# Kernel optimization log

Measured on AMD Instinct MI355X. Metric: run time of the kernel, lower is better.

The kernel has to match this reference:

```python
import jax, jax.numpy as jnp
import numpy as np


def _to_complex(x):
    # trailing axis holds (real, imag)
    return x[..., 0] + 1j * x[..., 1]


def _nufft2c(img, omega, csm):
    """Exact type-2 non-uniform DFT with coil sensitivities (reference for nufft2c_torch).

    img:   (H, W) real or complex image
    omega: (2, M) k-space coords in cycles/pixel, in [-0.5, 0.5]
    csm:   (C, H, W) complex coil sensitivity maps
    returns (C, M) complex k-space, centered & orthonormal-style 1/sqrt(HW) scaling.
    """
    H, W = img.shape
    y = jnp.arange(H, dtype=jnp.float32) - H / 2.0  # centered pixel coords
    z = jnp.arange(W, dtype=jnp.float32) - W / 2.0
    ey = jnp.exp(-2j * jnp.pi * omega[0][:, None] * y[None, :])  # (M, H)
    ez = jnp.exp(-2j * jnp.pi * omega[1][:, None] * z[None, :])  # (M, W)
    sim = csm * img[None, :, :].astype(csm.dtype)                # (C, H, W)
    tmp = jnp.einsum('chw,mw->cmh', sim, ez)                     # (C, M, H)
    k = jnp.einsum('cmh,mh->cm', tmp, ey) / np.float32(np.sqrt(H * W))
    return k


def setup_inputs() -> dict:
    key = jax.random.key(0)
    k0, k1, k2, k3, k4 = jax.random.split(key, 5)
    H = W = 300
    C = 4       # coils
    M = 4096    # non-Cartesian k-space samples
    img_pred = jax.random.normal(k0, (H, W, 1), jnp.float32)
    kdata = jax.random.normal(k1, (1, C, M, 2), jnp.float32)
    all_omega = jax.random.uniform(k2, (1, 2, M), jnp.float32) - 0.5  # cycles/pixel
    all_dcomp = jax.random.uniform(k3, (1, M), jnp.float32)
    all_csm = jax.random.normal(k4, (C, H, W, 2), jnp.float32)
    return {
        'img_pred': img_pred,
        'kdata': kdata,
        'all_omega': all_omega,
        'all_dcomp': all_dcomp,
        'all_csm': all_csm,
    }


def reference(img_pred, kdata, all_omega, all_dcomp, all_csm):
    Ncontrast = 1
    csm = _to_complex(all_csm)   # (C, H, W)
    kd = _to_complex(kdata)      # (Ncontrast, C, M)
    two_pi = jnp.float32(2.0 * np.pi)
    # radial k-space weighting, (Ncontrast, M)
    weight = jnp.sqrt((all_omega[:, 0, :] * two_pi) ** 2 +
                      (all_omega[:, 1, :] * two_pi) ** 2) + 1.0
    loss = jnp.float32(0.0)
    for ii in range(Ncontrast):
        img = img_pred[:, :, ii]                       # (H, W)
        ksp = _nufft2c(img, all_omega[ii], csm)        # (C, M)
        d = weight[ii][None, :] * (ksp - kd[ii])       # weighted complex residual
        # MSELoss over view_as_real == mean over all real & imag components
        loss = loss + jnp.mean(jnp.stack([d.real, d.imag]) ** 2)
    return loss
```

## Files before the change

### kernel.cpp

```cpp
#include <hip/hip_runtime.h>
#include <math.h>

#define HH 300
#define WW 300
#define CC 4
#define MM 4096
#define KP 640
#define CSTRIDE 384
#define MP (CC*CSTRIDE)
#define NP 8192
#define BK 128
#define NRB (MP/128)

typedef __attribute__((ext_vector_type(4))) float f32x4;
typedef __attribute__((ext_vector_type(4))) int int4v;
typedef __attribute__((ext_vector_type(8))) int int8v;
typedef const __attribute__((address_space(1))) void g_void;
typedef __attribute__((address_space(3))) void l_void;

#define TWO_PI 6.283185307179586f

__device__ __forceinline__ float aval(const float* img, const float* csm,
                                      int c, int h, int k) {
    if (k >= 2 * WW) return 0.0f;
    int w = (k < WW) ? k : k - WW;
    float im = img[h * WW + w];
    const float* cs = csm + (((size_t)c * HH + h) * WW + w) * 2;
    return ((k < WW) ? cs[0] : cs[1]) * im;
}

__device__ __forceinline__ float bval(const float* omega, int n, int k) {
    if (k >= 2 * WW) return 0.0f;
    int m = n & (MM - 1);
    int part = n >> 12;
    int w = (k < WW) ? k : k - WW;
    float om1 = omega[MM + m];
    float s, c;
    __sincosf(TWO_PI * om1 * (float)(w - 150), &s, &c);
    float ezr = c, ezi = -s;
    return (part == 0) ? ((k < WW) ? ezr : -ezi) : ((k < WW) ? ezi : ezr);
}

__global__ __launch_bounds__(256) void prep_kernel(
    const float* __restrict__ img, const float* __restrict__ csm,
    const float* __restrict__ omega, ushort* __restrict__ A,
    ushort* __restrict__ B, float* __restrict__ out)
{
    const int bid = blockIdx.x;
    if (bid == 0 && threadIdx.x == 0) out[0] = 0.0f;
    const int ABLK = (MP * KP / 2) / 256;
    if (bid < ABLK) {
        int idx = bid * 256 + threadIdx.x;
        int row = idx / (KP / 2);
        int k   = (idx - row * (KP / 2)) * 2;
        int c = row / CSTRIDE;
        int h = row - c * CSTRIDE;
        float v0 = 0.0f, v1 = 0.0f;
        if (h < HH) { v0 = aval(img, csm, c, h, k); v1 = aval(img, csm, c, h, k + 1); }
        int pk = __builtin_amdgcn_cvt_pk_fp8_f32(v0, v1, 0, false);
        A[idx] = (ushort)pk;
    } else {
        int idx = (bid - ABLK) * 256 + threadIdx.x;
        int n = idx / (KP / 2);
        int k = (idx - n * (KP / 2)) * 2;
        float v0 = bval(omega, n, k);
        float v1 = bval(omega, n, k + 1);
        int pk = __builtin_amdgcn_cvt_pk_fp8_f32(v0, v1, 0, false);
        B[idx] = (ushort)pk;
    }
}

__global__ __launch_bounds__(256) void gemm_kernel(
    const unsigned char* __restrict__ A, const unsigned char* __restrict__ B,
    const float* __restrict__ omega, float2* __restrict__ P)
{
    __shared__ unsigned char As[128 * BK];
    __shared__ unsigned char Bs[128 * BK];
    __shared__ float2 red[128];

    const int t    = threadIdx.x;
    const int wave = t >> 6;
    const int ln   = t & 63;
    const int row0 = blockIdx.y * 128;
    const int col0 = blockIdx.x * 128;
    const int wr = wave >> 1, wc = wave & 1;
    const int lr = ln & 15;
    const int lq = ln >> 4;

    if (t < 128) red[t] = make_float2(0.0f, 0.0f);

    const int srow  = t >> 3;
    const int cphys = (t >> 1) & 3;
    const int half  = t & 1;
    const int sgoff = ((cphys ^ (srow & 3)) << 5) + (half << 4);

    f32x4 acc[4][4] = {};

    for (int k0 = 0; k0 < KP; k0 += BK) {
        #pragma unroll
        for (int p = 0; p < 4; ++p) {
            const unsigned char* gA = A + (size_t)(row0 + p * 32 + srow) * KP + k0 + sgoff;
            const unsigned char* gB = B + (size_t)(col0 + p * 32 + srow) * KP + k0 + sgoff;
            __builtin_amdgcn_global_load_lds((g_void*)gA, (l_void*)(As + p * 4096 + t * 16), 16, 0, 0);
            __builtin_amdgcn_global_load_lds((g_void*)gB, (l_void*)(Bs + p * 4096 + t * 16), 16, 0, 0);
        }
        __syncthreads();

        int8v a[4], b[4];
        #pragma unroll
        for (int i = 0; i < 4; ++i) {
            const int r = wr * 64 + i * 16 + lr;
            const unsigned char* pA = As + r * BK + ((lq ^ (lr & 3)) << 5);
            int4v lo = *(const int4v*)pA;
            int4v hi = *(const int4v*)(pA + 16);
            a[i] = __builtin_shufflevector(lo, hi, 0, 1, 2, 3, 4, 5, 6, 7);
        }
        #pragma unroll
        for (int j = 0; j < 4; ++j) {
            const int r = wc * 64 + j * 16 + lr;
            const unsigned char* pB = Bs + r * BK + ((lq ^ (lr & 3)) << 5);
            int4v lo = *(const int4v*)pB;
            int4v hi = *(const int4v*)(pB + 16);
            b[j] = __builtin_shufflevector(lo, hi, 0, 1, 2, 3, 4, 5, 6, 7);
        }
        #pragma unroll
        for (int i = 0; i < 4; ++i)
            #pragma unroll
            for (int j = 0; j < 4; ++j)
                acc[i][j] = __builtin_amdgcn_mfma_scale_f32_16x16x128_f8f6f4(
                    a[i], b[j], acc[i][j], 0, 0,
                    0, 0x7f7f7f7f, 0, 0x7f7f7f7f);
        __syncthreads();
    }

    const int c  = row0 / CSTRIDE;
    const int h0 = row0 - c * CSTRIDE;

    #pragma unroll
    for (int j = 0; j < 4; ++j) {
        const int jcol = wc * 64 + j * 16 + lr;
        const int m = (col0 + jcol) & (MM - 1);
        const float om0 = omega[m];
        float ss, sc;
        __sincosf(TWO_PI * om0, &ss, &sc);
        const float str = sc, sti = -ss;
        float pr = 0.0f, pi = 0.0f;
        #pragma unroll
        for (int i = 0; i < 4; ++i) {
            const int hb = h0 + wr * 64 + i * 16 + lq * 4;
            float sn, cs;
            __sincosf(TWO_PI * om0 * (float)(hb - 150), &sn, &cs);
            float er = cs, ei = -sn;
            #pragma unroll
            for (int r = 0; r < 4; ++r) {
                const float v = acc[i][j][r];
                pr = fmaf(v, er, pr);
                pi = fmaf(v, ei, pi);
                float nr = er * str - ei * sti;
                ei = er * sti + ei * str;
                er = nr;
            }
        }
        pr += __shfl_down(pr, 32); pi += __shfl_down(pi, 32);
        pr += __shfl_down(pr, 16); pi += __shfl_down(pi, 16);
        if (lq == 0) {
            atomicAdd(&red[jcol].x, pr);
            atomicAdd(&red[jcol].y, pi);
        }
    }
    __syncthreads();

    if (t < 128) {
        const int rb = row0 >> 7;
        P[(size_t)rb * NP + col0 + t] = red[t];
    }
}

__global__ __launch_bounds__(256) void loss_kernel(
    const float2* __restrict__ P, const float* __restrict__ kdata,
    const float* __restrict__ omega, float* __restrict__ out)
{
    const int t = blockIdx.x * 256 + threadIdx.x;
    const int c = t >> 12;
    const int m = t & (MM - 1);

    float kr = 0.0f, ki = 0.0f;
    #pragma unroll
    for (int q = 0; q < 3; ++q) {
        const int rb = 3 * c + q;
        float2 p0 = P[(size_t)rb * NP + m];
        float2 p1 = P[(size_t)rb * NP + m + MM];
        kr += p0.x - p1.y;
        ki += p0.y + p1.x;
    }
    kr *= (1.0f / 300.0f);
    ki *= (1.0f / 300.0f);

    const float om0 = omega[m];
    const float om1 = omega[MM + m];
    const size_t kidx = ((size_t)c * MM + m) * 2;
    const float kdr = kdata[kidx];
    const float kdi = kdata[kidx + 1];
    const float w0 = om0 * TWO_PI, w1 = om1 * TWO_PI;
    const float wg = sqrtf(w0 * w0 + w1 * w1) + 1.0f;
    const float dr = wg * (kr - kdr);
    const float di = wg * (ki - kdi);
    float val = (dr * dr + di * di) * (1.0f / (2.0f * CC * MM));

    #pragma unroll
    for (int off = 32; off > 0; off >>= 1) val += __shfl_down(val, off);
    if ((threadIdx.x & 63) == 0) atomicAdd(out, val);
}

extern "C" void kernel_launch(void* const* d_in, const int* in_sizes, int n_in,
                              void* d_out, int out_size, void* d_ws, size_t ws_size,
                              hipStream_t stream) {
    const float* img   = (const float*)d_in[0];
    const float* kdata = (const float*)d_in[1];
    const float* omega = (const float*)d_in[2];
    const float* csm   = (const float*)d_in[4];
    float* out = (float*)d_out;

    unsigned char* Aws = (unsigned char*)d_ws;
    unsigned char* Bws = (unsigned char*)d_ws + (1u << 20);
    float2*        Pws = (float2*)((char*)d_ws + (8u << 20));

    const int ablk = (MP * KP / 2) / 256;
    const int bblk = (NP * KP / 2) / 256;
    prep_kernel<<<ablk + bblk, 256, 0, stream>>>(img, csm, omega,
                                                 (ushort*)Aws, (ushort*)Bws, out);
    gemm_kernel<<<dim3(NP / 128, MP / 128), 256, 0, stream>>>(Aws, Bws, omega, Pws);
    loss_kernel<<<(CC * MM) / 256, 256, 0, stream>>>(Pws, kdata, omega, out);
}
```

Measured before the change: 91.56 us.

## Fuse loss into GEMM via last-block reduction, dedupe B prep sincos, remap blocks per XCD

The separate loss kernel is removed. The last GEMM block to finish, found with an atomic counter and threadfence, now reduces all partial products and writes the loss, which saves a launch and the output atomics. B-matrix prep computes each sincos once and writes all four real/imag variants of both parts, so transcendental work drops by about 4x. The GEMM grid is flattened to 1D and remapped so blocks on the same XCD share column tiles for L2 locality. The cost is a serial tail where a single block reduces 16K elements.

```diff
diff --git a/kernel.cpp b/kernel.cpp
--- a/kernel.cpp
+++ b/kernel.cpp
@@ -11,6 +11,7 @@
 #define NP 8192
 #define BK 128
 #define NRB (MP/128)
+#define NBLK ((NP/128)*(MP/128))
 
 typedef __attribute__((ext_vector_type(4))) float f32x4;
 typedef __attribute__((ext_vector_type(4))) int int4v;
@@ -29,25 +30,13 @@
     return ((k < WW) ? cs[0] : cs[1]) * im;
 }
 
-__device__ __forceinline__ float bval(const float* omega, int n, int k) {
-    if (k >= 2 * WW) return 0.0f;
-    int m = n & (MM - 1);
-    int part = n >> 12;
-    int w = (k < WW) ? k : k - WW;
-    float om1 = omega[MM + m];
-    float s, c;
-    __sincosf(TWO_PI * om1 * (float)(w - 150), &s, &c);
-    float ezr = c, ezi = -s;
-    return (part == 0) ? ((k < WW) ? ezr : -ezi) : ((k < WW) ? ezi : ezr);
-}
-
 __global__ __launch_bounds__(256) void prep_kernel(
     const float* __restrict__ img, const float* __restrict__ csm,
     const float* __restrict__ omega, ushort* __restrict__ A,
-    ushort* __restrict__ B, float* __restrict__ out)
+    unsigned char* __restrict__ B, int* __restrict__ counter)
 {
     const int bid = blockIdx.x;
-    if (bid == 0 && threadIdx.x == 0) out[0] = 0.0f;
+    if (bid == 0 && threadIdx.x == 0) *counter = 0;
     const int ABLK = (MP * KP / 2) / 256;
     if (bid < ABLK) {
         int idx = bid * 256 + threadIdx.x;
@@ -61,28 +50,52 @@
         A[idx] = (ushort)pk;
     } else {
         int idx = (bid - ABLK) * 256 + threadIdx.x;
-        int n = idx / (KP / 2);
-        int k = (idx - n * (KP / 2)) * 2;
-        float v0 = bval(omega, n, k);
-        float v1 = bval(omega, n, k + 1);
-        int pk = __builtin_amdgcn_cvt_pk_fp8_f32(v0, v1, 0, false);
-        B[idx] = (ushort)pk;
+        int m  = idx / 160;
+        int wp = idx - m * 160;
+        unsigned char* r0 = B + (size_t)m * KP;
+        unsigned char* r1 = B + (size_t)(m + MM) * KP;
+        if (wp < 150) {
+            int w = wp * 2;
+            float om1 = omega[MM + m];
+            float s0, c0, s1, c1;
+            __sincosf(TWO_PI * om1 * (float)(w - 150), &s0, &c0);
+            __sincosf(TWO_PI * om1 * (float)(w - 149), &s1, &c1);
+            ushort rr = (ushort)__builtin_amdgcn_cvt_pk_fp8_f32(c0, c1, 0, false);
+            ushort ii = (ushort)__builtin_amdgcn_cvt_pk_fp8_f32(-s0, -s1, 0, false);
+            ushort ni = (ushort)__builtin_amdgcn_cvt_pk_fp8_f32(s0, s1, 0, false);
+            *(ushort*)(r0 + w)       = rr;
+            *(ushort*)(r0 + WW + w)  = ni;
+            *(ushort*)(r1 + w)       = ii;
+            *(ushort*)(r1 + WW + w)  = rr;
+        } else {
+            int z = (wp - 150) * 4;
+            *(unsigned int*)(r0 + 600 + z) = 0u;
+            *(unsigned int*)(r1 + 600 + z) = 0u;
+        }
     }
 }
 
 __global__ __launch_bounds__(256) void gemm_kernel(
     const unsigned char* __restrict__ A, const unsigned char* __restrict__ B,
-    const float* __restrict__ omega, float2* __restrict__ P)
+    const float* __restrict__ omega, const float* __restrict__ kdata,
+    float2* __restrict__ P, int* __restrict__ counter, float* __restrict__ out)
 {
     __shared__ unsigned char As[128 * BK];
     __shared__ unsigned char Bs[128 * BK];
     __shared__ float2 red[128];
+    __shared__ float wred[4];
+    __shared__ int lastflag;
 
     const int t    = threadIdx.x;
     const int wave = t >> 6;
     const int ln   = t & 63;
-    const int row0 = blockIdx.y * 128;
-    const int col0 = blockIdx.x * 128;
+
+    const int bid = blockIdx.x;
+    const int xcd = bid & 7;
+    const int sub = bid >> 3;
+    const int row0 = (sub >> 3) * 128;
+    const int col0 = (xcd * 8 + (sub & 7)) * 128;
+
     const int wr = wave >> 1, wc = wave & 1;
     const int lr = ln & 15;
     const int lq = ln >> 4;
@@ -174,42 +187,48 @@
         const int rb = row0 >> 7;
         P[(size_t)rb * NP + col0 + t] = red[t];
     }
-}
-
-__global__ __launch_bounds__(256) void loss_kernel(
-    const float2* __restrict__ P, const float* __restrict__ kdata,
-    const float* __restrict__ omega, float* __restrict__ out)
-{
-    const int t = blockIdx.x * 256 + threadIdx.x;
-    const int c = t >> 12;
-    const int m = t & (MM - 1);
-
-    float kr = 0.0f, ki = 0.0f;
+    __syncthreads();
+
+    if (t == 0) {
+        __threadfence();
+        int old = atomicAdd(counter, 1);
+        lastflag = (old == NBLK - 1);
+    }
+    __syncthreads();
+    if (!lastflag) return;
+    __threadfence();
+
+    float vsum = 0.0f;
+    for (int idx = t; idx < CC * MM; idx += 256) {
+        const int cc = idx >> 12;
+        const int m  = idx & (MM - 1);
+        float kr = 0.0f, ki = 0.0f;
+        #pragma unroll
+        for (int q = 0; q < 3; ++q) {
+            const int rb = 3 * cc + q;
+            float2 p0 = P[(size_t)rb * NP + m];
+            float2 p1 = P[(size_t)rb * NP + m + MM];
+            kr += p0.x - p1.y;
+            ki += p0.y + p1.x;
+        }
+        kr *= (1.0f / 300.0f);
+        ki *= (1.0f / 300.0f);
+        const float o0 = omega[m];
+        const float o1 = omega[MM + m];
+        const size_t kidx = ((size_t)cc * MM + m) * 2;
+        const float kdr = kdata[kidx];
+        const float kdi = kdata[kidx + 1];
+        const float w0 = o0 * TWO_PI, w1 = o1 * TWO_PI;
+        const float wg = sqrtf(w0 * w0 + w1 * w1) + 1.0f;
+        const float dr = wg * (kr - kdr);
+        const float di = wg * (ki - kdi);
+        vsum += (dr * dr + di * di) * (1.0f / (2.0f * CC * MM));
+    }
     #pragma unroll
-    for (int q = 0; q < 3; ++q) {
-        const int rb = 3 * c + q;
-        float2 p0 = P[(size_t)rb * NP + m];
-        float2 p1 = P[(size_t)rb * NP + m + MM];
-        kr += p0.x - p1.y;
-        ki += p0.y + p1.x;
-    }
-    kr *= (1.0f / 300.0f);
-    ki *= (1.0f / 300.0f);
-
-    const float om0 = omega[m];
-    const float om1 = omega[MM + m];
-    const size_t kidx = ((size_t)c * MM + m) * 2;
-    const float kdr = kdata[kidx];
-    const float kdi = kdata[kidx + 1];
-    const float w0 = om0 * TWO_PI, w1 = om1 * TWO_PI;
-    const float wg = sqrtf(w0 * w0 + w1 * w1) + 1.0f;
-    const float dr = wg * (kr - kdr);
-    const float di = wg * (ki - kdi);
-    float val = (dr * dr + di * di) * (1.0f / (2.0f * CC * MM));
-
-    #pragma unroll
-    for (int off = 32; off > 0; off >>= 1) val += __shfl_down(val, off);
-    if ((threadIdx.x & 63) == 0) atomicAdd(out, val);
+    for (int off = 32; off > 0; off >>= 1) vsum += __shfl_down(vsum, off);
+    if (ln == 0) wred[wave] = vsum;
+    __syncthreads();
+    if (t == 0) out[0] = wred[0] + wred[1] + wred[2] + wred[3];
 }
 
 extern "C" void kernel_launch(void* const* d_in, const int* in_sizes, int n_in,
@@ -224,11 +243,11 @@
     unsigned char* Aws = (unsigned char*)d_ws;
     unsigned char* Bws = (unsigned char*)d_ws + (1u << 20);
     float2*        Pws = (float2*)((char*)d_ws + (8u << 20));
+    int*           cnt = (int*)((char*)d_ws + (16u << 20));
 
     const int ablk = (MP * KP / 2) / 256;
-    const int bblk = (NP * KP / 2) / 256;
+    const int bblk = (MM * 160) / 256;
     prep_kernel<<<ablk + bblk, 256, 0, stream>>>(img, csm, omega,
-                                                 (ushort*)Aws, (ushort*)Bws, out);
-    gemm_kernel<<<dim3(NP / 128, MP / 128), 256, 0, stream>>>(Aws, Bws, omega, Pws);
-    loss_kernel<<<(CC * MM) / 256, 256, 0, stream>>>(Pws, kdata, omega, out);
-}
+                                                 (ushort*)Aws, Bws, cnt);
+    gemm_kernel<<<NBLK, 256, 0, stream>>>(Aws, Bws, omega, kdata, Pws, cnt, out);
+}
```

After: 148.4 us. 1.62x slower.
